# Performance work log

Hardware: AMD Instinct MI355X
Metric: run time of the kernel (lower is better)

## Reference

```python
import jax, jax.numpy as jnp
from jax import lax
import numpy as np

DIM = 256
QK = 256          # qk_dim defaults to dim
HEADS = 8
NWIN = 7
TOPK = 4
KS = 3            # side_dwconv


def setup_inputs() -> dict:
    key = jax.random.key(0)
    ks = jax.random.split(key, 8)
    B, H, W = 1, 112, 112
    s = lambda d: 1.0 / np.sqrt(d)
    return {
        "x": jax.random.normal(ks[0], (B, H, W, DIM), jnp.float32),
        # fused qkv linear: dim -> qk + qk + dim
        "w_qkv": jax.random.normal(ks[1], (DIM, 2 * QK + DIM), jnp.float32) * s(DIM),
        "b_qkv": jnp.zeros((2 * QK + DIM,), jnp.float32),
        # output projection
        "w_o": jax.random.normal(ks[2], (DIM, DIM), jnp.float32) * s(DIM),
        "b_o": jnp.zeros((DIM,), jnp.float32),
        # depthwise 3x3 lepe conv (HWIO with I=1, groups=dim)
        "lepe_w": jax.random.normal(ks[3], (KS, KS, 1, DIM), jnp.float32) * s(KS * KS),
        "lepe_b": jnp.zeros((DIM,), jnp.float32),
    }


def _win2img(t, B, H, W, c):
    # (B, p2, h, w, c) windows -> (B, H, W, c) image
    hw, ww = H // NWIN, W // NWIN
    t = t.reshape(B, NWIN, NWIN, hw, ww, c)
    return t.transpose(0, 1, 3, 2, 4, 5).reshape(B, H, W, c)


def reference(x, w_qkv, b_qkv, w_o, b_o, lepe_w, lepe_b):
    B, H, W, C = x.shape
    hw, ww = H // NWIN, W // NWIN
    p2, w2 = NWIN * NWIN, hw * ww
    hd_q, hd_v = QK // HEADS, DIM // HEADS
    scale = QK ** (-0.5)

    # partition into windows: (B, p2, hw, ww, C)
    xp = x.reshape(B, NWIN, hw, NWIN, ww, C).transpose(0, 1, 3, 2, 4, 5)
    xp = xp.reshape(B, p2, hw, ww, C)

    qkv = xp @ w_qkv + b_qkv
    q, kv = qkv[..., :QK], qkv[..., QK:]          # (B,p2,hw,ww,QK), (...,QK+DIM)

    q_pix = q.reshape(B, p2, w2, QK)
    kv_pix = kv.reshape(B, p2, w2, QK + DIM)      # identity kv_down

    # region-level routing (detached in original since diff_routing=False)
    q_win = lax.stop_gradient(q.mean((2, 3)))     # (B,p2,QK)
    k_win = lax.stop_gradient(kv[..., :QK].mean((2, 3)))
    logit = (q_win * scale) @ jnp.swapaxes(k_win, -1, -2)   # (B,p2,p2)
    top_logit, top_idx = lax.top_k(logit, TOPK)             # (B,p2,TOPK)
    r_weight = jax.nn.softmax(top_logit, axis=-1)           # unused: mul_weight='none'

    # gather top-k regions' KV: (B, p2, TOPK, w2, QK+DIM)
    kv_sel = jax.vmap(lambda kvb, idxb: kvb[idxb])(kv_pix, top_idx)

    k_sel = kv_sel[..., :QK].reshape(B, p2, TOPK * w2, HEADS, hd_q)
    v_sel = kv_sel[..., QK:].reshape(B, p2, TOPK * w2, HEADS, hd_v)
    qh = q_pix.reshape(B, p2, w2, HEADS, hd_q)

    attn = jnp.einsum('bpqhc,bpkhc->bphqk', qh * scale, k_sel)
    attn = jax.nn.softmax(attn, axis=-1)
    out = jnp.einsum('bphqk,bpkhc->bpqhc', attn, v_sel).reshape(B, p2, hw, ww, DIM)
    out = _win2img(out, B, H, W, DIM)

    # lepe: depthwise conv over v in image layout
    v_img = _win2img(kv[..., QK:], B, H, W, DIM)
    lepe = lax.conv_general_dilated(
        v_img, lepe_w, (1, 1), 'SAME',
        dimension_numbers=('NHWC', 'HWIO', 'NHWC'),
        feature_group_count=DIM) + lepe_b

    return (out + lepe) @ w_o + b_o
```

## Files before the change

### kernel.cpp

```cpp
#include <hip/hip_runtime.h>
#include <math.h>


typedef __bf16 bf16x8 __attribute__((ext_vector_type(8)));
typedef __bf16 bf16x4 __attribute__((ext_vector_type(4)));
typedef float f32x4 __attribute__((ext_vector_type(4)));

__global__ __launch_bounds__(64)
void pack1(const float* __restrict__ x, const float* __restrict__ w_qkv,
           const float* __restrict__ w_o, __bf16* __restrict__ xbf,
           __bf16* __restrict__ wtq, __bf16* __restrict__ wto) {
    const int b = blockIdx.x;
    const int t = threadIdx.x;
    if (b < 12544) {
        int p = b >> 8, pix = b & 255;
        int hh = (p / 7) * 16 + (pix >> 4);
        int ww = (p % 7) * 16 + (pix & 15);
        const float* src = x + ((size_t)(hh * 112 + ww)) * 256 + t * 4;
        float4 v = *(const float4*)src;
        bf16x4 o;
        o[0] = (__bf16)v.x; o[1] = (__bf16)v.y; o[2] = (__bf16)v.z; o[3] = (__bf16)v.w;
        *(bf16x4*)(xbf + (size_t)b * 256 + t * 4) = o;
    } else if (b < 12544 + 768) {
        int n = b - 12544;
        int k = t * 4;
        bf16x4 o;
        o[0] = (__bf16)w_qkv[(k + 0) * 768 + n];
        o[1] = (__bf16)w_qkv[(k + 1) * 768 + n];
        o[2] = (__bf16)w_qkv[(k + 2) * 768 + n];
        o[3] = (__bf16)w_qkv[(k + 3) * 768 + n];
        *(bf16x4*)(wtq + (size_t)n * 256 + k) = o;
    } else {
        int n = b - 12544 - 768;
        int k = t * 4;
        bf16x4 o;
        o[0] = (__bf16)w_o[(k + 0) * 256 + n];
        o[1] = (__bf16)w_o[(k + 1) * 256 + n];
        o[2] = (__bf16)w_o[(k + 2) * 256 + n];
        o[3] = (__bf16)w_o[(k + 3) * 256 + n];
        *(bf16x4*)(wto + (size_t)n * 256 + k) = o;
    }
}

template<int QKV>
__global__ __launch_bounds__(256)
void gemm_bf16(const __bf16* __restrict__ A,
               const __bf16* __restrict__ Wt,
               const float* __restrict__ bias,
               float* __restrict__ C, int N,
               __bf16* __restrict__ Qp,
               __bf16* __restrict__ Kp,
               __bf16* __restrict__ vbf,
               __bf16* __restrict__ Vt) {
    const int t = threadIdx.x & 63;
    const int wv = threadIdx.x >> 6;
    const int l16 = t & 15, quad = t >> 4;
    const int m0 = blockIdx.x * 64;
    const int n0 = blockIdx.y * 128 + wv * 32;

    __shared__ __bf16 Vs[128][72];

    f32x4 acc[2][4];
#pragma unroll
    for (int km = 0; km < 2; km++)
#pragma unroll
        for (int nt = 0; nt < 4; nt++) acc[km][nt] = (f32x4){0.f, 0.f, 0.f, 0.f};

#pragma unroll
    for (int ks = 0; ks < 8; ks++) {
        bf16x8 Af[2], Bf[4];
#pragma unroll
        for (int km = 0; km < 2; km++)
            Af[km] = *(const bf16x8*)(Wt + (size_t)(n0 + km * 16 + l16) * 256 + ks * 32 + quad * 8);
#pragma unroll
        for (int nt = 0; nt < 4; nt++)
            Bf[nt] = *(const bf16x8*)(A + (size_t)(m0 + nt * 16 + l16) * 256 + ks * 32 + quad * 8);
#pragma unroll
        for (int km = 0; km < 2; km++)
#pragma unroll
            for (int nt = 0; nt < 4; nt++)
                acc[km][nt] = __builtin_amdgcn_mfma_f32_16x16x32_bf16(
                    Af[km], Bf[nt], acc[km][nt], 0, 0, 0);
    }

#pragma unroll
    for (int km = 0; km < 2; km++) {
        const int n = n0 + km * 16 + quad * 4;
        float4 b4 = *(const float4*)(bias + n);
#pragma unroll
        for (int nt = 0; nt < 4; nt++) {
            const int m = m0 + nt * 16 + l16;
            float v0 = acc[km][nt][0] + b4.x;
            float v1 = acc[km][nt][1] + b4.y;
            float v2 = acc[km][nt][2] + b4.z;
            float v3 = acc[km][nt][3] + b4.w;
            if (QKV == 0) {
                float4 o = {v0, v1, v2, v3};
                *(float4*)(C + (size_t)m * N + n) = o;
            } else {
                const int p = m >> 8, pix = m & 255;
                if (n0 < 256) {
                    const float s = 1.0f / 16.0f;
                    int h = n >> 5, cc = n & 31;
                    bf16x4 o;
                    o[0] = (__bf16)(v0 * s); o[1] = (__bf16)(v1 * s);
                    o[2] = (__bf16)(v2 * s); o[3] = (__bf16)(v3 * s);
                    *(bf16x4*)(Qp + ((size_t)((p * 8 + h) * 256 + pix)) * 32 + cc) = o;
                } else if (n0 < 512) {
                    int n2 = n - 256;
                    int h = n2 >> 5, cc = n2 & 31;
                    bf16x4 o;
                    o[0] = (__bf16)v0; o[1] = (__bf16)v1;
                    o[2] = (__bf16)v2; o[3] = (__bf16)v3;
                    *(bf16x4*)(Kp + ((size_t)((p * 8 + h) * 256 + pix)) * 32 + cc) = o;
                } else {
                    int n2 = n - 512;
                    int imgrow = ((p / 7) * 16 + (pix >> 4)) * 112 + (p % 7) * 16 + (pix & 15);
                    bf16x4 o;
                    o[0] = (__bf16)v0; o[1] = (__bf16)v1;
                    o[2] = (__bf16)v2; o[3] = (__bf16)v3;
                    *(bf16x4*)(vbf + (size_t)imgrow * 256 + n2) = o;
                    const int cbase = wv * 32 + km * 16 + quad * 4;
                    const int pb = nt * 16 + l16;
                    Vs[cbase + 0][pb] = o[0];
                    Vs[cbase + 1][pb] = o[1];
                    Vs[cbase + 2][pb] = o[2];
                    Vs[cbase + 3][pb] = o[3];
                }
            }
        }
    }

    if (QKV == 1 && blockIdx.y >= 4) {
        __syncthreads();
        const int p_ = m0 >> 8, qt_ = (m0 >> 6) & 3;
        const int vb = blockIdx.y * 128 - 512;
#pragma unroll
        for (int rep = 0; rep < 4; rep++) {
            int id = rep * 256 + threadIdx.x;
            int row = id >> 3, c8 = (id & 7) * 8;
            int hh = (vb + row) >> 5, c32 = (vb + row) & 31;
            bf16x8 val = *(const bf16x8*)&Vs[row][c8];
            *(bf16x8*)(Vt + ((size_t)((p_ * 8 + hh) * 32 + c32)) * 256 + qt_ * 64 + c8) = val;
        }
    }
}

__global__ __launch_bounds__(256)
void win_means(const __bf16* __restrict__ Qp,
               const __bf16* __restrict__ Kp,
               float* __restrict__ q_win, float* __restrict__ k_win) {
    const int b = blockIdx.x;
    const int p = b >> 3, h = b & 7;
    const int t = threadIdx.x;
    const int c8 = (t & 3) * 8;
    const int r0 = t >> 2;
    float aq[8], ak[8];
#pragma unroll
    for (int j = 0; j < 8; j++) { aq[j] = 0.f; ak[j] = 0.f; }
#pragma unroll
    for (int rg = 0; rg < 4; rg++) {
        const int r = rg * 64 + r0;
        bf16x8 q = *(const bf16x8*)(Qp + ((size_t)(b * 256 + r)) * 32 + c8);
        bf16x8 k = *(const bf16x8*)(Kp + ((size_t)(b * 256 + r)) * 32 + c8);
#pragma unroll
        for (int j = 0; j < 8; j++) { aq[j] += (float)q[j]; ak[j] += (float)k[j]; }
    }
    __shared__ float Sq[256][8], Sk[256][8];
#pragma unroll
    for (int j = 0; j < 8; j++) { Sq[t][j] = aq[j]; Sk[t][j] = ak[j]; }
    __syncthreads();
    if (t < 32) {
        const int grp = t >> 3, cj = t & 7;
        float sq = 0.f, sk = 0.f;
        for (int i = 0; i < 64; i++) {
            sq += Sq[i * 4 + grp][cj];
            sk += Sk[i * 4 + grp][cj];
        }
        q_win[p * 256 + h * 32 + t] = sq * (1.f / 256.f);
        k_win[p * 256 + h * 32 + t] = sk * (1.f / 256.f);
    }
}

__global__ __launch_bounds__(64)
void routing_topk(const float* __restrict__ q_win,
                  const float* __restrict__ k_win,
                  int* __restrict__ top_idx) {
    const int r = blockIdx.x;
    const int j = threadIdx.x;
    __shared__ float vals[64];

    float d = -1e30f;
    if (j < 49) {
        const float4* qp = (const float4*)(q_win + r * 256);
        const float4* kp = (const float4*)(k_win + j * 256);
        float s = 0.f;
#pragma unroll
        for (int c = 0; c < 64; c++) {
            float4 a = qp[c], b = kp[c];
            s += a.x * b.x + a.y * b.y + a.z * b.z + a.w * b.w;
        }
        d = s;
    }
    vals[j] = d;
    __syncthreads();
    if (j == 0) {
        float bv0 = -1e30f, bv1 = -1e30f, bv2 = -1e30f, bv3 = -1e30f;
        int bi0 = 0, bi1 = 0, bi2 = 0, bi3 = 0;
        for (int q = 0; q < 49; q++) {
            float v = vals[q];
            if (v > bv0) {
                bv3 = bv2; bi3 = bi2; bv2 = bv1; bi2 = bi1; bv1 = bv0; bi1 = bi0;
                bv0 = v; bi0 = q;
            } else if (v > bv1) {
                bv3 = bv2; bi3 = bi2; bv2 = bv1; bi2 = bi1; bv1 = v; bi1 = q;
            } else if (v > bv2) {
                bv3 = bv2; bi3 = bi2; bv2 = v; bi2 = q;
            } else if (v > bv3) {
                bv3 = v; bi3 = q;
            }
        }
        top_idx[r * 4 + 0] = bi0;
        top_idx[r * 4 + 1] = bi1;
        top_idx[r * 4 + 2] = bi2;
        top_idx[r * 4 + 3] = bi3;
    }
}

#define PLDS_PITCH 68
#define HALO_PITCH 36

__global__ __launch_bounds__(64)
void attn_mfma(const __bf16* __restrict__ Qp,
               const __bf16* __restrict__ Kp,
               const __bf16* __restrict__ Vt,
               const int* __restrict__ top_idx,
               const __bf16* __restrict__ vbf,
               const float* __restrict__ lw,
               const float* __restrict__ lb,
               __bf16* __restrict__ prebf) {
    const int bb = blockIdx.x;
    const int qt = bb / 392;
    const int ph = bb - qt * 392;
    const int p = ph >> 3;
    const int h = ph & 7;
    const int t = threadIdx.x;
    const int l16 = t & 15, quad = t >> 4;

    __shared__ unsigned short Plds[64 * PLDS_PITCH];
    __shared__ __bf16 Hs[108 * HALO_PITCH];

    bf16x8 Qf[4];
#pragma unroll
    for (int nt = 0; nt < 4; nt++)
        Qf[nt] = *(const bf16x8*)(Qp + ((size_t)((p * 8 + h) * 256 + qt * 64 + nt * 16 + l16)) * 32 + quad * 8);

    float lstate[4] = {0.f, 0.f, 0.f, 0.f};
    f32x4 O[2][4];
#pragma unroll
    for (int mt = 0; mt < 2; mt++)
#pragma unroll
        for (int nt = 0; nt < 4; nt++) O[mt][nt] = (f32x4){0.f, 0.f, 0.f, 0.f};

    int sels[4];
#pragma unroll
    for (int s = 0; s < 4; s++) sels[s] = top_idx[p * 4 + s];

    bf16x8 Kf[4];
    {
        const __bf16* Kb = Kp + ((size_t)(sels[0] * 8 + h)) * 8192;
#pragma unroll
        for (int km = 0; km < 4; km++)
            Kf[km] = *(const bf16x8*)(Kb + (size_t)(km * 16 + l16) * 32 + quad * 8);
    }

    for (int kc = 0; kc < 16; kc++) {
        const int sel = sels[kc >> 2];
        const int kbase = (kc & 3) * 64;

        const __bf16* Vb = Vt + ((size_t)(sel * 8 + h)) * 8192;
        bf16x8 Vf[2][2];
#pragma unroll
        for (int kstep = 0; kstep < 2; kstep++)
#pragma unroll
            for (int mt = 0; mt < 2; mt++)
                Vf[kstep][mt] = *(const bf16x8*)(Vb + (size_t)(mt * 16 + l16) * 256 + kbase + kstep * 32 + quad * 8);

        const int kcn = (kc < 15) ? kc + 1 : 15;
        const __bf16* Kbn = Kp + ((size_t)(sels[kcn >> 2] * 8 + h)) * 8192;
        const int kbn = (kcn & 3) * 64;
        bf16x8 Kn[4];
#pragma unroll
        for (int km = 0; km < 4; km++)
            Kn[km] = *(const bf16x8*)(Kbn + (size_t)(kbn + km * 16 + l16) * 32 + quad * 8);

#pragma unroll
        for (int nt = 0; nt < 4; nt++) {
            f32x4 S[4];
#pragma unroll
            for (int km = 0; km < 4; km++)
                S[km] = __builtin_amdgcn_mfma_f32_16x16x32_bf16(
                    Kf[km], Qf[nt], (f32x4){0.f, 0.f, 0.f, 0.f}, 0, 0, 0);

            float rs = 0.f;
#pragma unroll
            for (int km = 0; km < 4; km++) {
                union { unsigned short u[4]; ushort4 v; } pk;
#pragma unroll
                for (int r = 0; r < 4; r++) {
                    float pv = __expf(S[km][r]);
                    rs += pv;
                    pk.u[r] = __builtin_bit_cast(unsigned short, (__bf16)pv);
                }
                *(ushort4*)&Plds[(nt * 16 + l16) * PLDS_PITCH + km * 16 + quad * 4] = pk.v;
            }
            rs += __shfl_xor(rs, 16);
            rs += __shfl_xor(rs, 32);
            lstate[nt] += rs;
        }

#pragma unroll
        for (int kstep = 0; kstep < 2; kstep++) {
#pragma unroll
            for (int nt = 0; nt < 4; nt++) {
                int idx = (nt * 16 + l16) * PLDS_PITCH + kstep * 32 + quad * 8;
                union { ushort4 u4[2]; bf16x8 v; } pu;
                pu.u4[0] = *(const ushort4*)&Plds[idx];
                pu.u4[1] = *(const ushort4*)&Plds[idx + 4];
#pragma unroll
                for (int mt = 0; mt < 2; mt++)
                    O[mt][nt] = __builtin_amdgcn_mfma_f32_16x16x32_bf16(
                        Vf[kstep][mt], pu.v, O[mt][nt], 0, 0, 0);
            }
        }

#pragma unroll
        for (int km = 0; km < 4; km++) Kf[km] = Kn[km];
    }

    const int pr = p / 7, pc = p % 7;
    for (int i = t; i < 108; i += 64) {
        int hy = i / 18, hx = i - hy * 18;
        int gy = pr * 16 + qt * 4 - 1 + hy;
        int gx = pc * 16 - 1 + hx;
        union { bf16x4 v4[8]; bf16x8 v8[4]; uint4 q[4]; } u;
        u.q[0] = (uint4){0u, 0u, 0u, 0u};
        u.q[1] = (uint4){0u, 0u, 0u, 0u};
        u.q[2] = (uint4){0u, 0u, 0u, 0u};
        u.q[3] = (uint4){0u, 0u, 0u, 0u};
        if (gy >= 0 && gy < 112 && gx >= 0 && gx < 112) {
            const __bf16* src = vbf + ((size_t)(gy * 112 + gx)) * 256 + h * 32;
            u.v8[0] = *(const bf16x8*)src;
            u.v8[1] = *(const bf16x8*)(src + 8);
            u.v8[2] = *(const bf16x8*)(src + 16);
            u.v8[3] = *(const bf16x8*)(src + 24);
        }
#pragma unroll
        for (int j = 0; j < 8; j++)
            *(bf16x4*)&Hs[i * HALO_PITCH + j * 4] = u.v4[j];
    }
    __syncthreads();

#pragma unroll
    for (int mt = 0; mt < 2; mt++) {
        const int c = h * 32 + mt * 16 + quad * 4;
        const float4 lbv = *(const float4*)(lb + c);
        float a0[4], a1[4], a2[4], a3[4];
#pragma unroll
        for (int nt = 0; nt < 4; nt++) {
            a0[nt] = lbv.x; a1[nt] = lbv.y; a2[nt] = lbv.z; a3[nt] = lbv.w;
        }
#pragma unroll
        for (int dh = 0; dh < 3; dh++)
#pragma unroll
            for (int dw = 0; dw < 3; dw++) {
                const float4 w4 = *(const float4*)(lw + (dh * 3 + dw) * 256 + c);
#pragma unroll
                for (int nt = 0; nt < 4; nt++) {
                    const bf16x4 v4 = *(const bf16x4*)&Hs[((nt + dh) * 18 + l16 + dw) * HALO_PITCH + mt * 16 + quad * 4];
                    a0[nt] += (float)v4[0] * w4.x;
                    a1[nt] += (float)v4[1] * w4.y;
                    a2[nt] += (float)v4[2] * w4.z;
                    a3[nt] += (float)v4[3] * w4.w;
                }
            }
#pragma unroll
        for (int nt = 0; nt < 4; nt++) {
            const float inv = 1.f / lstate[nt];
            bf16x4 ob;
            ob[0] = (__bf16)(O[mt][nt][0] * inv + a0[nt]);
            ob[1] = (__bf16)(O[mt][nt][1] * inv + a1[nt]);
            ob[2] = (__bf16)(O[mt][nt][2] * inv + a2[nt]);
            ob[3] = (__bf16)(O[mt][nt][3] * inv + a3[nt]);
            const int himg = pr * 16 + qt * 4 + nt, wimg = pc * 16 + l16;
            *(bf16x4*)(prebf + ((size_t)(himg * 112 + wimg)) * 256 + c) = ob;
        }
    }
}

extern "C" void kernel_launch(void* const* d_in, const int* in_sizes, int n_in,
                              void* d_out, int out_size, void* d_ws, size_t ws_size,
                              hipStream_t stream) {
    const float* x      = (const float*)d_in[0];
    const float* w_qkv  = (const float*)d_in[1];
    const float* b_qkv  = (const float*)d_in[2];
    const float* w_o    = (const float*)d_in[3];
    const float* b_o    = (const float*)d_in[4];
    const float* lepe_w = (const float*)d_in[5];
    const float* lepe_b = (const float*)d_in[6];
    float* out = (float*)d_out;

    char* w = (char*)d_ws;
    __bf16* Qp    = (__bf16*)w; w += 6422528;
    __bf16* Kp    = (__bf16*)w; w += 6422528;
    __bf16* vbf   = (__bf16*)w; w += 6422528;
    __bf16* Vt    = (__bf16*)w; w += 6422528;
    __bf16* xbf   = (__bf16*)w;
    __bf16* prebf = (__bf16*)w; w += 6422528;
    __bf16* wtq   = (__bf16*)w; w += 393216;
    __bf16* wto   = (__bf16*)w; w += 131072;
    float* q_win   = (float*)w; w += 12544 * 4;
    float* k_win   = (float*)w; w += 12544 * 4;
    int*   top_idx = (int*)w;

    pack1<<<12544 + 768 + 256, 64, 0, stream>>>(x, w_qkv, w_o, xbf, wtq, wto);
    gemm_bf16<1><<<dim3(196, 6), 256, 0, stream>>>(xbf, wtq, b_qkv,
                                                   nullptr, 0, Qp, Kp, vbf, Vt);
    win_means<<<392, 256, 0, stream>>>(Qp, Kp, q_win, k_win);
    routing_topk<<<49, 64, 0, stream>>>(q_win, k_win, top_idx);
    attn_mfma<<<392 * 4, 64, 0, stream>>>(Qp, Kp, Vt, top_idx,
                                          vbf, lepe_w, lepe_b, prebf);
    gemm_bf16<0><<<dim3(196, 2), 256, 0, stream>>>(prebf, wto, b_o,
                                                   out, 256, nullptr, nullptr, nullptr, nullptr);
}
```

Before: 188.7 us.

## Fuse x bf16 packing and window-mean reduction into QKV GEMM

The QKV GEMM now reads the fp32 input directly in window order and converts it to bf16 in registers, so the separate per-pixel pack pass and its bf16 copy of x are gone. The GEMM epilogue also reduces q/k columns per window and atomically accumulates them into a small sum buffer, which replaces the win_means kernel. Routing then adds the bias back to the means. The cost is a memset launch, atomics in the GEMM epilogue, and fp32 global loads of A that are twice as wide inside the GEMM.

```diff
diff --git a/kernel.cpp b/kernel.cpp
--- a/kernel.cpp
+++ b/kernel.cpp
@@ -7,22 +7,12 @@
 typedef float f32x4 __attribute__((ext_vector_type(4)));
 
 __global__ __launch_bounds__(64)
-void pack1(const float* __restrict__ x, const float* __restrict__ w_qkv,
-           const float* __restrict__ w_o, __bf16* __restrict__ xbf,
+void pack1(const float* __restrict__ w_qkv, const float* __restrict__ w_o,
            __bf16* __restrict__ wtq, __bf16* __restrict__ wto) {
     const int b = blockIdx.x;
     const int t = threadIdx.x;
-    if (b < 12544) {
-        int p = b >> 8, pix = b & 255;
-        int hh = (p / 7) * 16 + (pix >> 4);
-        int ww = (p % 7) * 16 + (pix & 15);
-        const float* src = x + ((size_t)(hh * 112 + ww)) * 256 + t * 4;
-        float4 v = *(const float4*)src;
-        bf16x4 o;
-        o[0] = (__bf16)v.x; o[1] = (__bf16)v.y; o[2] = (__bf16)v.z; o[3] = (__bf16)v.w;
-        *(bf16x4*)(xbf + (size_t)b * 256 + t * 4) = o;
-    } else if (b < 12544 + 768) {
-        int n = b - 12544;
+    if (b < 768) {
+        int n = b;
         int k = t * 4;
         bf16x4 o;
         o[0] = (__bf16)w_qkv[(k + 0) * 768 + n];
@@ -31,7 +21,7 @@
         o[3] = (__bf16)w_qkv[(k + 3) * 768 + n];
         *(bf16x4*)(wtq + (size_t)n * 256 + k) = o;
     } else {
-        int n = b - 12544 - 768;
+        int n = b - 768;
         int k = t * 4;
         bf16x4 o;
         o[0] = (__bf16)w_o[(k + 0) * 256 + n];
@@ -45,13 +35,15 @@
 template<int QKV>
 __global__ __launch_bounds__(256)
 void gemm_bf16(const __bf16* __restrict__ A,
+               const float* __restrict__ Xf,
                const __bf16* __restrict__ Wt,
                const float* __restrict__ bias,
                float* __restrict__ C, int N,
                __bf16* __restrict__ Qp,
                __bf16* __restrict__ Kp,
                __bf16* __restrict__ vbf,
-               __bf16* __restrict__ Vt) {
+               __bf16* __restrict__ Vt,
+               float* __restrict__ qksum) {
     const int t = threadIdx.x & 63;
     const int wv = threadIdx.x >> 6;
     const int l16 = t & 15, quad = t >> 4;
@@ -60,6 +52,20 @@
 
     __shared__ __bf16 Vs[128][72];
 
+    const float* aptrF[4];
+    const __bf16* aptrB[4];
+#pragma unroll
+    for (int nt = 0; nt < 4; nt++) {
+        const int m = m0 + nt * 16 + l16;
+        if (QKV == 1) {
+            int pix = m & 255, p_ = m >> 8;
+            int row = ((p_ / 7) * 16 + (pix >> 4)) * 112 + (p_ % 7) * 16 + (pix & 15);
+            aptrF[nt] = Xf + (size_t)row * 256;
+        } else {
+            aptrB[nt] = A + (size_t)m * 256;
+        }
+    }
+
     f32x4 acc[2][4];
 #pragma unroll
     for (int km = 0; km < 2; km++)
@@ -73,14 +79,49 @@
         for (int km = 0; km < 2; km++)
             Af[km] = *(const bf16x8*)(Wt + (size_t)(n0 + km * 16 + l16) * 256 + ks * 32 + quad * 8);
 #pragma unroll
-        for (int nt = 0; nt < 4; nt++)
-            Bf[nt] = *(const bf16x8*)(A + (size_t)(m0 + nt * 16 + l16) * 256 + ks * 32 + quad * 8);
+        for (int nt = 0; nt < 4; nt++) {
+            if (QKV == 1) {
+                const float* s = aptrF[nt] + ks * 32 + quad * 8;
+                float4 fa = *(const float4*)s;
+                float4 fb = *(const float4*)(s + 4);
+                bf16x8 r;
+                r[0] = (__bf16)fa.x; r[1] = (__bf16)fa.y;
+                r[2] = (__bf16)fa.z; r[3] = (__bf16)fa.w;
+                r[4] = (__bf16)fb.x; r[5] = (__bf16)fb.y;
+                r[6] = (__bf16)fb.z; r[7] = (__bf16)fb.w;
+                Bf[nt] = r;
+            } else {
+                Bf[nt] = *(const bf16x8*)(aptrB[nt] + ks * 32 + quad * 8);
+            }
+        }
 #pragma unroll
         for (int km = 0; km < 2; km++)
 #pragma unroll
             for (int nt = 0; nt < 4; nt++)
                 acc[km][nt] = __builtin_amdgcn_mfma_f32_16x16x32_bf16(
                     Af[km], Bf[nt], acc[km][nt], 0, 0, 0);
+    }
+
+    if (QKV == 1 && blockIdx.y < 4) {
+        const int p = m0 >> 8;
+#pragma unroll
+        for (int km = 0; km < 2; km++) {
+            f32x4 rs;
+#pragma unroll
+            for (int r = 0; r < 4; r++)
+                rs[r] = acc[km][0][r] + acc[km][1][r] + acc[km][2][r] + acc[km][3][r];
+#pragma unroll
+            for (int off = 1; off < 16; off <<= 1) {
+#pragma unroll
+                for (int r = 0; r < 4; r++) rs[r] += __shfl_xor(rs[r], off);
+            }
+            if (l16 == 0) {
+                const int n = n0 + km * 16 + quad * 4;
+#pragma unroll
+                for (int r = 0; r < 4; r++)
+                    atomicAdd(&qksum[p * 512 + n + r], rs[r]);
+            }
+        }
     }
 
 #pragma unroll
@@ -146,59 +187,28 @@
     }
 }
 
-__global__ __launch_bounds__(256)
-void win_means(const __bf16* __restrict__ Qp,
-               const __bf16* __restrict__ Kp,
-               float* __restrict__ q_win, float* __restrict__ k_win) {
-    const int b = blockIdx.x;
-    const int p = b >> 3, h = b & 7;
-    const int t = threadIdx.x;
-    const int c8 = (t & 3) * 8;
-    const int r0 = t >> 2;
-    float aq[8], ak[8];
-#pragma unroll
-    for (int j = 0; j < 8; j++) { aq[j] = 0.f; ak[j] = 0.f; }
-#pragma unroll
-    for (int rg = 0; rg < 4; rg++) {
-        const int r = rg * 64 + r0;
-        bf16x8 q = *(const bf16x8*)(Qp + ((size_t)(b * 256 + r)) * 32 + c8);
-        bf16x8 k = *(const bf16x8*)(Kp + ((size_t)(b * 256 + r)) * 32 + c8);
-#pragma unroll
-        for (int j = 0; j < 8; j++) { aq[j] += (float)q[j]; ak[j] += (float)k[j]; }
-    }
-    __shared__ float Sq[256][8], Sk[256][8];
-#pragma unroll
-    for (int j = 0; j < 8; j++) { Sq[t][j] = aq[j]; Sk[t][j] = ak[j]; }
-    __syncthreads();
-    if (t < 32) {
-        const int grp = t >> 3, cj = t & 7;
-        float sq = 0.f, sk = 0.f;
-        for (int i = 0; i < 64; i++) {
-            sq += Sq[i * 4 + grp][cj];
-            sk += Sk[i * 4 + grp][cj];
-        }
-        q_win[p * 256 + h * 32 + t] = sq * (1.f / 256.f);
-        k_win[p * 256 + h * 32 + t] = sk * (1.f / 256.f);
-    }
-}
-
 __global__ __launch_bounds__(64)
-void routing_topk(const float* __restrict__ q_win,
-                  const float* __restrict__ k_win,
+void routing_topk(const float* __restrict__ qksum,
+                  const float* __restrict__ b_qkv,
                   int* __restrict__ top_idx) {
     const int r = blockIdx.x;
     const int j = threadIdx.x;
     __shared__ float vals[64];
+    const float inv = 1.0f / 256.0f;
 
     float d = -1e30f;
     if (j < 49) {
-        const float4* qp = (const float4*)(q_win + r * 256);
-        const float4* kp = (const float4*)(k_win + j * 256);
         float s = 0.f;
 #pragma unroll
-        for (int c = 0; c < 64; c++) {
-            float4 a = qp[c], b = kp[c];
-            s += a.x * b.x + a.y * b.y + a.z * b.z + a.w * b.w;
+        for (int c = 0; c < 256; c += 4) {
+            float4 qs = *(const float4*)(qksum + r * 512 + c);
+            float4 ks = *(const float4*)(qksum + j * 512 + 256 + c);
+            float4 bq = *(const float4*)(b_qkv + c);
+            float4 bk = *(const float4*)(b_qkv + 256 + c);
+            s += (qs.x * inv + bq.x) * (ks.x * inv + bk.x);
+            s += (qs.y * inv + bq.y) * (ks.y * inv + bk.y);
+            s += (qs.z * inv + bq.z) * (ks.z * inv + bk.z);
+            s += (qs.w * inv + bq.w) * (ks.w * inv + bk.w);
         }
         d = s;
     }
@@ -415,21 +425,19 @@
     __bf16* Kp    = (__bf16*)w; w += 6422528;
     __bf16* vbf   = (__bf16*)w; w += 6422528;
     __bf16* Vt    = (__bf16*)w; w += 6422528;
-    __bf16* xbf   = (__bf16*)w;
     __bf16* prebf = (__bf16*)w; w += 6422528;
     __bf16* wtq   = (__bf16*)w; w += 393216;
     __bf16* wto   = (__bf16*)w; w += 131072;
-    float* q_win   = (float*)w; w += 12544 * 4;
-    float* k_win   = (float*)w; w += 12544 * 4;
+    float* qksum   = (float*)w; w += 49 * 512 * 4;
     int*   top_idx = (int*)w;
 
-    pack1<<<12544 + 768 + 256, 64, 0, stream>>>(x, w_qkv, w_o, xbf, wtq, wto);
-    gemm_bf16<1><<<dim3(196, 6), 256, 0, stream>>>(xbf, wtq, b_qkv,
-                                                   nullptr, 0, Qp, Kp, vbf, Vt);
-    win_means<<<392, 256, 0, stream>>>(Qp, Kp, q_win, k_win);
-    routing_topk<<<49, 64, 0, stream>>>(q_win, k_win, top_idx);
+    hipMemsetAsync(qksum, 0, 49 * 512 * sizeof(float), stream);
+    pack1<<<768 + 256, 64, 0, stream>>>(w_qkv, w_o, wtq, wto);
+    gemm_bf16<1><<<dim3(196, 6), 256, 0, stream>>>(nullptr, x, wtq, b_qkv,
+                                                   nullptr, 0, Qp, Kp, vbf, Vt, qksum);
+    routing_topk<<<49, 64, 0, stream>>>(qksum, b_qkv, top_idx);
     attn_mfma<<<392 * 4, 64, 0, stream>>>(Qp, Kp, Vt, top_idx,
                                           vbf, lepe_w, lepe_b, prebf);
-    gemm_bf16<0><<<dim3(196, 2), 256, 0, stream>>>(prebf, wto, b_o,
-                                                   out, 256, nullptr, nullptr, nullptr, nullptr);
+    gemm_bf16<0><<<dim3(196, 2), 256, 0, stream>>>(prebf, nullptr, wto, b_o,
+                                                   out, 256, nullptr, nullptr, nullptr, nullptr, nullptr);
 }
```

Measured after the change: 204.0 us. +8.1%, slower.
